# Kernel tuning notes

Hardware: AMD Instinct MI355X
Metric: run time of the kernel (lower is better)

The kernel has to match this reference:

```python
import jax, jax.numpy as jnp
import numpy as np

NEG_SLOPE = 0.2
EPS = 1e-16

N_NODES = 50000
N_EDGES = 800000
IN_CH = 128
HEADS = 4
OUT_CH = 32


def setup_inputs() -> dict:
    key = jax.random.key(0)
    k1, k2, k3, k4, k5 = jax.random.split(key, 5)
    x = jax.random.normal(k1, (N_NODES, IN_CH), dtype=jnp.float32)
    edge_index = jax.random.randint(k2, (2, N_EDGES), 0, N_NODES, dtype=jnp.int64)
    # Glorot-ish scaling for stability
    W = jax.random.normal(k3, (IN_CH, HEADS * OUT_CH), dtype=jnp.float32) / np.sqrt(IN_CH)
    att_src = jax.random.normal(k4, (HEADS, OUT_CH), dtype=jnp.float32) / np.sqrt(OUT_CH)
    att_dst = jax.random.normal(k5, (HEADS, OUT_CH), dtype=jnp.float32) / np.sqrt(OUT_CH)
    bias = jnp.zeros((HEADS * OUT_CH,), dtype=jnp.float32)
    return {"x": x, "edge_index": edge_index, "W": W,
            "att_src": att_src, "att_dst": att_dst, "bias": bias}


def reference(x, edge_index, W, att_src, att_dst, bias):
    N = x.shape[0]
    H, C = att_src.shape

    # PyG GATConv default: add self-loops
    self_loop = jnp.arange(N, dtype=edge_index.dtype)
    src = jnp.concatenate([edge_index[0], self_loop])  # [E+N]
    dst = jnp.concatenate([edge_index[1], self_loop])  # [E+N]

    # Linear transform, split heads: [N, H, C]
    h = (x @ W).reshape(N, H, C)

    # Per-node attention logits: [N, H]
    a_src = jnp.sum(h * att_src[None], axis=-1)
    a_dst = jnp.sum(h * att_dst[None], axis=-1)

    # Per-edge logits with LeakyReLU: [E+N, H]
    e = a_src[src] + a_dst[dst]
    e = jnp.where(e >= 0, e, NEG_SLOPE * e)

    # Segment softmax over destination-node neighborhoods
    e_max = jax.ops.segment_max(e, dst, num_segments=N)  # [N, H]
    e_exp = jnp.exp(e - e_max[dst])
    denom = jax.ops.segment_sum(e_exp, dst, num_segments=N)  # [N, H]
    alpha = e_exp / (denom[dst] + EPS)  # [E+N, H]

    # Weighted scatter-aggregate of messages: [N, H, C]
    msgs = h[src] * alpha[:, :, None]
    out = jax.ops.segment_sum(msgs, dst, num_segments=N)

    out = out.reshape(N, H * C) + bias  # concat heads + bias
    return jax.nn.relu(out)  # wrapper activation (dropout=0 is identity)
```

## Files before the change

kernel.cpp:

```cpp
#include <hip/hip_runtime.h>
#include <hip/hip_bf16.h>
#include <math.h>

#define NEG_SLOPE 0.2f
#define EPS_F 1e-16f
#define PCAP 4096
#define NPMAX 512

typedef float f32x4 __attribute__((ext_vector_type(4)));
typedef short bf16x8 __attribute__((ext_vector_type(8)));

__device__ __forceinline__ unsigned int pk2bf(float a, float b) {
    unsigned int ua = __float_as_uint(a), ub = __float_as_uint(b);
    ua = (ua + 0x7fffu + ((ua >> 16) & 1u)) >> 16;
    ub = (ub + 0x7fffu + ((ub >> 16) & 1u)) >> 16;
    return ua | (ub << 16);
}
__device__ __forceinline__ unsigned short f2bf(float f) {
    unsigned int u = __float_as_uint(f);
    return (unsigned short)((u + 0x7fffu + ((u >> 16) & 1u)) >> 16);
}
__device__ __forceinline__ float bf_lo(unsigned int p) { return __uint_as_float(p << 16); }
__device__ __forceinline__ float bf_hi(unsigned int p) { return __uint_as_float(p & 0xffff0000u); }

__global__ __launch_bounds__(256)
void k_front(const unsigned int* __restrict__ eidx,
             int* __restrict__ pcnt, unsigned int* __restrict__ rec, int E, int npart,
             const float* __restrict__ W,
             const float* __restrict__ att_src, const float* __restrict__ att_dst,
             unsigned short* __restrict__ Wtb, int nPB) {
    __shared__ int hist[NPMAX];
    __shared__ int base[NPMAX];
    __shared__ int sflag;
    int t = threadIdx.x;

    if ((int)blockIdx.x < nPB) {
        if (t < 64) {
            unsigned int v = eidx[2 * t + 1];
            #pragma unroll
            for (int m = 1; m <= 32; m <<= 1) v |= __shfl_xor(v, m);
            if (t == 0) sflag = (v == 0u) ? 1 : 0;
        }
        for (int p = t; p < npart; p += 256) hist[p] = 0;
        __syncthreads();
        int flag = sflag;
        const uint2* e2p = (const uint2*)eidx;
        int e0 = blockIdx.x * 4096;
        int se[16], de[16];
        #pragma unroll
        for (int i = 0; i < 16; i++) {
            int idx = e0 + t + i * 256;
            de[i] = -1;
            if (idx < E) {
                if (flag) { se[i] = (int)e2p[idx].x; de[i] = (int)e2p[E + idx].x; }
                else      { se[i] = (int)eidx[idx];  de[i] = (int)eidx[E + idx]; }
                atomicAdd(&hist[de[i] >> 7], 1);
            }
        }
        __syncthreads();
        for (int p = t; p < npart; p += 256) {
            int c = hist[p];
            base[p] = c ? atomicAdd(&pcnt[p], c) : 0;
            hist[p] = 0;
        }
        __syncthreads();
        #pragma unroll
        for (int i = 0; i < 16; i++) {
            if (de[i] >= 0) {
                int p = de[i] >> 7;
                int r = atomicAdd(&hist[p], 1);
                int pos = base[p] + r;
                if (pos < PCAP)
                    rec[(size_t)p * PCAP + pos] =
                        ((unsigned int)se[i] << 7) | (unsigned int)(de[i] & 127);
            }
        }
    } else {
        int b = (int)blockIdx.x - nPB;
        if (b < 64) {
            int id = b * 256 + t;
            int k = id >> 7, col = id & 127;
            Wtb[col * 128 + k] = f2bf(W[id]);
        } else {
            int k4 = t >> 3, j = t & 7;
            const float* att = (j < 4) ? att_src : att_dst;
            int h = j & 3;
            #pragma unroll
            for (int kk = 0; kk < 4; kk++) {
                int k = k4 * 4 + kk;
                float s = 0.f;
                #pragma unroll
                for (int c = 0; c < 32; c++)
                    s = fmaf(W[k * 128 + h * 32 + c], att[h * 32 + c], s);
                Wtb[(128 + j) * 128 + k] = f2bf(s);
            }
            for (int idx = t; idx < 1024; idx += 256)
                Wtb[(136 + (idx >> 7)) * 128 + (idx & 127)] = 0;
        }
    }
}

__global__ __launch_bounds__(256)
void k_mid(const float* __restrict__ x, const unsigned short* __restrict__ Wtb,
           unsigned short* __restrict__ hb,
           float* __restrict__ a_src, float* __restrict__ a_dst, int N,
           const int* __restrict__ pcnt, const unsigned int* __restrict__ rec,
           unsigned int* __restrict__ srt, int* __restrict__ rowArr,
           int* __restrict__ degArr, int gb) {
    __shared__ __align__(16) char smem[53248];
    int t = threadIdx.x;

    if ((int)blockIdx.x < gb) {
        unsigned short* xlds = (unsigned short*)smem;
        unsigned short* wlds = (unsigned short*)(smem + 16384);
        int l = t & 63, w = t >> 6;
        int br = blockIdx.x * 64;

        #pragma unroll
        for (int i = 0; i < 9; i++) {
            int u = t + i * 256;
            uint4 v = *(const uint4*)(Wtb + u * 8);
            int row = u >> 4;
            int e8  = (u & 15) * 8;
            *(uint4*)&wlds[row * 128 + (e8 ^ ((row & 7) << 3))] = v;
        }
        {
            int row = t >> 2, kq = t & 3;
            int gr = br + row;
            const float* xp = x + (size_t)gr * 128 + kq * 32;
            #pragma unroll
            for (int j = 0; j < 4; j++) {
                uint4 pk = make_uint4(0u, 0u, 0u, 0u);
                if (gr < N) {
                    float4 v0 = *(const float4*)(xp + j * 8);
                    float4 v1 = *(const float4*)(xp + j * 8 + 4);
                    pk.x = pk2bf(v0.x, v0.y); pk.y = pk2bf(v0.z, v0.w);
                    pk.z = pk2bf(v1.x, v1.y); pk.w = pk2bf(v1.z, v1.w);
                }
                int e8 = kq * 32 + j * 8;
                *(uint4*)&xlds[row * 128 + (e8 ^ ((row & 7) << 3))] = pk;
            }
        }
        __syncthreads();

        bf16x8 a[4];
        int arow = w * 16 + (l & 15);
        int ae   = (l >> 4) * 8;
        #pragma unroll
        for (int kc = 0; kc < 4; kc++)
            a[kc] = *(const bf16x8*)&xlds[arow * 128 + ((kc * 32 + ae) ^ ((arow & 7) << 3))];

        int rowbase = br + w * 16 + (l >> 4) * 4;

        #pragma unroll
        for (int nb = 0; nb < 9; nb++) {
            int brow = nb * 16 + (l & 15);
            f32x4 c = {0.f, 0.f, 0.f, 0.f};
            #pragma unroll
            for (int kc = 0; kc < 4; kc++) {
                bf16x8 bfr = *(const bf16x8*)&wlds[brow * 128 + ((kc * 32 + ae) ^ ((brow & 7) << 3))];
                c = __builtin_amdgcn_mfma_f32_16x16x32_bf16(a[kc], bfr, c, 0, 0, 0);
            }
            if (nb < 8) {
                #pragma unroll
                for (int r = 0; r < 4; r++) {
                    float v  = c[r];
                    float vo = __shfl_xor(v, 1);
                    int row = rowbase + r;
                    if (row < N && (l & 1) == 0)
                        *(unsigned int*)&hb[(size_t)row * 128 + nb * 16 + (l & 15)] = pk2bf(v, vo);
                }
            } else {
                int j = l & 15;
                #pragma unroll
                for (int r = 0; r < 4; r++) {
                    int row = rowbase + r;
                    if (row < N && j < 8) {
                        if (j < 4) a_src[row * 4 + j]     = c[r];
                        else       a_dst[row * 4 + j - 4] = c[r];
                    }
                }
            }
        }
    } else {
        int* hist = (int*)smem;
        int* offs = hist + 128;
        int* cur  = offs + 128;
        unsigned int* ssort = (unsigned int*)(smem + 1536);
        int p = (int)blockIdx.x - gb;
        if (t < 128) { hist[t] = 0; cur[t] = 0; }
        __syncthreads();
        int cnt = min(pcnt[p], PCAP);
        const unsigned int* rb = rec + (size_t)p * PCAP;
        for (int i = t; i < cnt; i += 256) atomicAdd(&hist[rb[i] & 127], 1);
        __syncthreads();
        if (t < 128) offs[t] = hist[t];
        __syncthreads();
        #pragma unroll
        for (int off = 1; off < 128; off <<= 1) {
            int u = (t < 128 && t >= off) ? offs[t - off] : 0;
            __syncthreads();
            if (t < 128) offs[t] += u;
            __syncthreads();
        }
        for (int i = t; i < cnt; i += 256) {
            unsigned int r = rb[i];
            int n = r & 127;
            int pos = (offs[n] - hist[n]) + atomicAdd(&cur[n], 1);
            ssort[pos] = r >> 7;
        }
        __syncthreads();
        for (int i = t; i < cnt; i += 256) srt[(size_t)p * PCAP + i] = ssort[i];
        int node = (p << 7) + t;
        if (t < 128 && node < N) {
            rowArr[node] = p * PCAP + (offs[t] - hist[t]);
            degArr[node] = hist[t];
        }
    }
}

#define BATCH4(bk, j, ad, den, ax, ay)                                          \
    {                                                                            \
        int s0=(int)bk[j], s1=(int)bk[j+1], s2=(int)bk[j+2], s3=(int)bk[j+3];    \
        float a0=a_src[s0*4+head], a1=a_src[s1*4+head];                          \
        float a2=a_src[s2*4+head], a3=a_src[s3*4+head];                          \
        unsigned int p0=*(const unsigned int*)&hb[(size_t)s0*128+c0];            \
        unsigned int p1=*(const unsigned int*)&hb[(size_t)s1*128+c0];            \
        unsigned int p2=*(const unsigned int*)&hb[(size_t)s2*128+c0];            \
        unsigned int p3=*(const unsigned int*)&hb[(size_t)s3*128+c0];            \
        float e0=a0+ad; e0=fmaxf(e0,NEG_SLOPE*e0); float w0=__expf(e0);          \
        float e1=a1+ad; e1=fmaxf(e1,NEG_SLOPE*e1); float w1=__expf(e1);          \
        float e2=a2+ad; e2=fmaxf(e2,NEG_SLOPE*e2); float w2=__expf(e2);          \
        float e3=a3+ad; e3=fmaxf(e3,NEG_SLOPE*e3); float w3=__expf(e3);          \
        den += (w0+w1)+(w2+w3);                                                  \
        ax = fmaf(w0,bf_lo(p0),ax); ay = fmaf(w0,bf_hi(p0),ay);                  \
        ax = fmaf(w1,bf_lo(p1),ax); ay = fmaf(w1,bf_hi(p1),ay);                  \
        ax = fmaf(w2,bf_lo(p2),ax); ay = fmaf(w2,bf_hi(p2),ay);                  \
        ax = fmaf(w3,bf_lo(p3),ax); ay = fmaf(w3,bf_hi(p3),ay);                  \
    }

#define ONEEDGE(bk, j, ad, den, ax, ay)                                          \
    {                                                                            \
        int s0=(int)bk[j];                                                       \
        float a0=a_src[s0*4+head];                                               \
        unsigned int p0=*(const unsigned int*)&hb[(size_t)s0*128+c0];            \
        float e0=a0+ad; e0=fmaxf(e0,NEG_SLOPE*e0); float w0=__expf(e0);          \
        den += w0;                                                               \
        ax = fmaf(w0,bf_lo(p0),ax); ay = fmaf(w0,bf_hi(p0),ay);                  \
    }

__global__ __launch_bounds__(256)
void k_aggregate(const unsigned int* __restrict__ srt, const int* __restrict__ rowArr,
                 const int* __restrict__ degArr,
                 const float* __restrict__ a_src, const float* __restrict__ a_dst,
                 const unsigned short* __restrict__ hb,
                 const float* __restrict__ bias,
                 float* __restrict__ out, int N) {
    int wave = threadIdx.x >> 6;
    int lane = threadIdx.x & 63;
    int c0 = lane * 2;
    int head = lane >> 4;
    int dA = blockIdx.x * 8 + wave * 2;
    int dB = dA + 1;
    if (dA >= N) return;
    bool vB = dB < N;

    float adA, denA, axA, ayA; const unsigned int* bkA; int gA;
    {
        adA = a_dst[dA * 4 + head];
        float es = a_src[dA * 4 + head] + adA;
        es = fmaxf(es, NEG_SLOPE * es);
        float w = __expf(es);
        unsigned int hp = *(const unsigned int*)&hb[(size_t)dA * 128 + c0];
        denA = w; axA = w * bf_lo(hp); ayA = w * bf_hi(hp);
        bkA = srt + rowArr[dA]; gA = degArr[dA];
    }
    float adB = 0.f, denB = 0.f, axB = 0.f, ayB = 0.f;
    const unsigned int* bkB = srt; int gB = 0;
    if (vB) {
        adB = a_dst[dB * 4 + head];
        float es = a_src[dB * 4 + head] + adB;
        es = fmaxf(es, NEG_SLOPE * es);
        float w = __expf(es);
        unsigned int hp = *(const unsigned int*)&hb[(size_t)dB * 128 + c0];
        denB = w; axB = w * bf_lo(hp); ayB = w * bf_hi(hp);
        bkB = srt + rowArr[dB]; gB = degArr[dB];
    }

    int jA = 0, jB = 0;
    while (jA + 4 <= gA && jB + 4 <= gB) {
        BATCH4(bkA, jA, adA, denA, axA, ayA);
        BATCH4(bkB, jB, adB, denB, axB, ayB);
        jA += 4; jB += 4;
    }
    while (jA + 4 <= gA) { BATCH4(bkA, jA, adA, denA, axA, ayA); jA += 4; }
    while (jB + 4 <= gB) { BATCH4(bkB, jB, adB, denB, axB, ayB); jB += 4; }
    while (jA < gA && jB < gB) {
        ONEEDGE(bkA, jA, adA, denA, axA, ayA);
        ONEEDGE(bkB, jB, adB, denB, axB, ayB);
        jA++; jB++;
    }
    for (; jA < gA; jA++) ONEEDGE(bkA, jA, adA, denA, axA, ayA);
    for (; jB < gB; jB++) ONEEDGE(bkB, jB, adB, denB, axB, ayB);

    float2 b2 = *(const float2*)&bias[c0];
    {
        float rden = 1.f / (denA + EPS_F);
        float ox = fmaxf(axA * rden + b2.x, 0.f);
        float oy = fmaxf(ayA * rden + b2.y, 0.f);
        *(float2*)&out[(size_t)dA * 128 + c0] = make_float2(ox, oy);
    }
    if (vB) {
        float rden = 1.f / (denB + EPS_F);
        float ox = fmaxf(axB * rden + b2.x, 0.f);
        float oy = fmaxf(ayB * rden + b2.y, 0.f);
        *(float2*)&out[(size_t)dB * 128 + c0] = make_float2(ox, oy);
    }
}

extern "C" void kernel_launch(void* const* d_in, const int* in_sizes, int n_in,
                              void* d_out, int out_size, void* d_ws, size_t ws_size,
                              hipStream_t stream) {
    const float* x        = (const float*)d_in[0];
    const unsigned int* e = (const unsigned int*)d_in[1];
    const float* W        = (const float*)d_in[2];
    const float* att_src  = (const float*)d_in[3];
    const float* att_dst  = (const float*)d_in[4];
    const float* bias     = (const float*)d_in[5];
    float* out            = (float*)d_out;

    int N = in_sizes[0] / 128;
    int E = in_sizes[1] / 2;
    int npart = (N + 127) >> 7;

    char* ws = (char*)d_ws;
    size_t off = 0;
    unsigned short* Wtb    = (unsigned short*)(ws + off); off += 144 * 128 * 2;
    unsigned short* hb     = (unsigned short*)(ws + off); off += (size_t)N * 128 * 2;
    float*          a_src  = (float*)(ws + off);          off += (size_t)N * 16;
    float*          a_dst  = (float*)(ws + off);          off += (size_t)N * 16;
    int*            rowArr = (int*)(ws + off);            off += (size_t)N * 4;
    int*            degArr = (int*)(ws + off);            off += (size_t)N * 4;
    int*            pcnt   = (int*)(ws + off);            off += (size_t)NPMAX * 4;
    unsigned int*   rec    = (unsigned int*)(ws + off);   off += (size_t)npart * PCAP * 4;
    unsigned int*   srt    = (unsigned int*)(ws + off);   off += (size_t)npart * PCAP * 4;

    int nPB = (E + 4095) / 4096;
    int gb  = (N + 63) / 64;

    hipMemsetAsync(pcnt, 0, (size_t)NPMAX * 4, stream);

    k_front<<<nPB + 65, 256, 0, stream>>>(e, pcnt, rec, E, npart,
                                          W, att_src, att_dst, Wtb, nPB);
    k_mid<<<gb + npart, 256, 0, stream>>>(x, Wtb, hb, a_src, a_dst, N,
                                          pcnt, rec, srt, rowArr, degArr, gb);
    k_aggregate<<<(N + 7) / 8, 256, 0, stream>>>(srt, rowArr, degArr,
                                                 a_src, a_dst, hb, bias, out, N);
}
```

Before: 80.98 us.

## Regroup kernels: fuse edge partitioning with GEMM, split prep and binning, use exp2

The weight preparation moves into its own small kernel. Edge partitioning now runs in the same launch as the x@W GEMM, and the per-partition counting sort becomes a separate kernel. The attention projection columns are pre-scaled by log2(e), so the aggregate kernel can call exp2f instead of __expf. This aims to overlap the memory-bound edge pass with the compute-bound GEMM, at the cost of one extra kernel launch; the bf16 rounding of the scaled logits changes slightly.

Result: slower. 87.71 us (+8.3%).

```diff
diff --git a/kernel.cpp b/kernel.cpp
--- a/kernel.cpp
+++ b/kernel.cpp
@@ -6,6 +6,7 @@
 #define EPS_F 1e-16f
 #define PCAP 4096
 #define NPMAX 512
+#define LOG2E 1.44269504088896f
 
 typedef float f32x4 __attribute__((ext_vector_type(4)));
 typedef short bf16x8 __attribute__((ext_vector_type(8)));
@@ -23,27 +24,54 @@
 __device__ __forceinline__ float bf_lo(unsigned int p) { return __uint_as_float(p << 16); }
 __device__ __forceinline__ float bf_hi(unsigned int p) { return __uint_as_float(p & 0xffff0000u); }
 
+__global__ void k_prep(const float* __restrict__ W,
+                       const float* __restrict__ att_src, const float* __restrict__ att_dst,
+                       unsigned short* __restrict__ Wtb) {
+    int b = blockIdx.x, t = threadIdx.x;
+    if (b < 64) {
+        int id = b * 256 + t;
+        int k = id >> 7, col = id & 127;
+        Wtb[col * 128 + k] = f2bf(W[id]);
+    } else {
+        int k4 = t >> 3, j = t & 7;
+        const float* att = (j < 4) ? att_src : att_dst;
+        int h = j & 3;
+        #pragma unroll
+        for (int kk = 0; kk < 4; kk++) {
+            int k = k4 * 4 + kk;
+            float s = 0.f;
+            #pragma unroll
+            for (int c = 0; c < 32; c++)
+                s = fmaf(W[k * 128 + h * 32 + c], att[h * 32 + c], s);
+            Wtb[(128 + j) * 128 + k] = f2bf(s * LOG2E);
+        }
+        for (int idx = t; idx < 1024; idx += 256)
+            Wtb[(136 + (idx >> 7)) * 128 + (idx & 127)] = 0;
+    }
+}
+
 __global__ __launch_bounds__(256)
-void k_front(const unsigned int* __restrict__ eidx,
-             int* __restrict__ pcnt, unsigned int* __restrict__ rec, int E, int npart,
-             const float* __restrict__ W,
-             const float* __restrict__ att_src, const float* __restrict__ att_dst,
-             unsigned short* __restrict__ Wtb, int nPB) {
-    __shared__ int hist[NPMAX];
-    __shared__ int base[NPMAX];
-    __shared__ int sflag;
+void k_pg(const unsigned int* __restrict__ eidx,
+          int* __restrict__ pcnt, unsigned int* __restrict__ rec, int E, int npart,
+          const float* __restrict__ x, const unsigned short* __restrict__ Wtb,
+          unsigned short* __restrict__ hb,
+          float* __restrict__ a_src, float* __restrict__ a_dst, int N, int nPB) {
+    __shared__ __align__(16) char smem[53248];
     int t = threadIdx.x;
 
     if ((int)blockIdx.x < nPB) {
+        int* hist = (int*)smem;
+        int* base = (int*)(smem + 2048);
+        int* sflagp = (int*)(smem + 4096);
         if (t < 64) {
             unsigned int v = eidx[2 * t + 1];
             #pragma unroll
             for (int m = 1; m <= 32; m <<= 1) v |= __shfl_xor(v, m);
-            if (t == 0) sflag = (v == 0u) ? 1 : 0;
+            if (t == 0) *sflagp = (v == 0u) ? 1 : 0;
         }
         for (int p = t; p < npart; p += 256) hist[p] = 0;
         __syncthreads();
-        int flag = sflag;
+        int flag = *sflagp;
         const uint2* e2p = (const uint2*)eidx;
         int e0 = blockIdx.x * 4096;
         int se[16], de[16];
@@ -76,45 +104,10 @@
             }
         }
     } else {
-        int b = (int)blockIdx.x - nPB;
-        if (b < 64) {
-            int id = b * 256 + t;
-            int k = id >> 7, col = id & 127;
-            Wtb[col * 128 + k] = f2bf(W[id]);
-        } else {
-            int k4 = t >> 3, j = t & 7;
-            const float* att = (j < 4) ? att_src : att_dst;
-            int h = j & 3;
-            #pragma unroll
-            for (int kk = 0; kk < 4; kk++) {
-                int k = k4 * 4 + kk;
-                float s = 0.f;
-                #pragma unroll
-                for (int c = 0; c < 32; c++)
-                    s = fmaf(W[k * 128 + h * 32 + c], att[h * 32 + c], s);
-                Wtb[(128 + j) * 128 + k] = f2bf(s);
-            }
-            for (int idx = t; idx < 1024; idx += 256)
-                Wtb[(136 + (idx >> 7)) * 128 + (idx & 127)] = 0;
-        }
-    }
-}
-
-__global__ __launch_bounds__(256)
-void k_mid(const float* __restrict__ x, const unsigned short* __restrict__ Wtb,
-           unsigned short* __restrict__ hb,
-           float* __restrict__ a_src, float* __restrict__ a_dst, int N,
-           const int* __restrict__ pcnt, const unsigned int* __restrict__ rec,
-           unsigned int* __restrict__ srt, int* __restrict__ rowArr,
-           int* __restrict__ degArr, int gb) {
-    __shared__ __align__(16) char smem[53248];
-    int t = threadIdx.x;
-
-    if ((int)blockIdx.x < gb) {
         unsigned short* xlds = (unsigned short*)smem;
         unsigned short* wlds = (unsigned short*)(smem + 16384);
         int l = t & 63, w = t >> 6;
-        int br = blockIdx.x * 64;
+        int br = ((int)blockIdx.x - nPB) * 64;
 
         #pragma unroll
         for (int i = 0; i < 9; i++) {
@@ -182,40 +175,45 @@
                 }
             }
         }
-    } else {
-        int* hist = (int*)smem;
-        int* offs = hist + 128;
-        int* cur  = offs + 128;
-        unsigned int* ssort = (unsigned int*)(smem + 1536);
-        int p = (int)blockIdx.x - gb;
-        if (t < 128) { hist[t] = 0; cur[t] = 0; }
-        __syncthreads();
-        int cnt = min(pcnt[p], PCAP);
-        const unsigned int* rb = rec + (size_t)p * PCAP;
-        for (int i = t; i < cnt; i += 256) atomicAdd(&hist[rb[i] & 127], 1);
-        __syncthreads();
-        if (t < 128) offs[t] = hist[t];
-        __syncthreads();
-        #pragma unroll
-        for (int off = 1; off < 128; off <<= 1) {
-            int u = (t < 128 && t >= off) ? offs[t - off] : 0;
-            __syncthreads();
-            if (t < 128) offs[t] += u;
-            __syncthreads();
-        }
-        for (int i = t; i < cnt; i += 256) {
-            unsigned int r = rb[i];
-            int n = r & 127;
-            int pos = (offs[n] - hist[n]) + atomicAdd(&cur[n], 1);
-            ssort[pos] = r >> 7;
-        }
-        __syncthreads();
-        for (int i = t; i < cnt; i += 256) srt[(size_t)p * PCAP + i] = ssort[i];
-        int node = (p << 7) + t;
-        if (t < 128 && node < N) {
-            rowArr[node] = p * PCAP + (offs[t] - hist[t]);
-            degArr[node] = hist[t];
-        }
+    }
+}
+
+__global__ __launch_bounds__(256)
+void k_bin2(const int* __restrict__ pcnt, const unsigned int* __restrict__ rec,
+            unsigned int* __restrict__ srt, int* __restrict__ rowArr,
+            int* __restrict__ degArr, int N) {
+    __shared__ int hist[128];
+    __shared__ int offs[128];
+    __shared__ int cur[128];
+    __shared__ unsigned int ssort[PCAP];
+    int p = blockIdx.x, t = threadIdx.x;
+    if (t < 128) { hist[t] = 0; cur[t] = 0; }
+    __syncthreads();
+    int cnt = min(pcnt[p], PCAP);
+    const unsigned int* rb = rec + (size_t)p * PCAP;
+    for (int i = t; i < cnt; i += 256) atomicAdd(&hist[rb[i] & 127], 1);
+    __syncthreads();
+    if (t < 128) offs[t] = hist[t];
+    __syncthreads();
+    #pragma unroll
+    for (int off = 1; off < 128; off <<= 1) {
+        int u = (t < 128 && t >= off) ? offs[t - off] : 0;
+        __syncthreads();
+        if (t < 128) offs[t] += u;
+        __syncthreads();
+    }
+    for (int i = t; i < cnt; i += 256) {
+        unsigned int r = rb[i];
+        int n = r & 127;
+        int pos = (offs[n] - hist[n]) + atomicAdd(&cur[n], 1);
+        ssort[pos] = r >> 7;
+    }
+    __syncthreads();
+    for (int i = t; i < cnt; i += 256) srt[(size_t)p * PCAP + i] = ssort[i];
+    int node = (p << 7) + t;
+    if (t < 128 && node < N) {
+        rowArr[node] = p * PCAP + (offs[t] - hist[t]);
+        degArr[node] = hist[t];
     }
 }
 
@@ -228,10 +226,10 @@
         unsigned int p1=*(const unsigned int*)&hb[(size_t)s1*128+c0];            \
         unsigned int p2=*(const unsigned int*)&hb[(size_t)s2*128+c0];            \
         unsigned int p3=*(const unsigned int*)&hb[(size_t)s3*128+c0];            \
-        float e0=a0+ad; e0=fmaxf(e0,NEG_SLOPE*e0); float w0=__expf(e0);          \
-        float e1=a1+ad; e1=fmaxf(e1,NEG_SLOPE*e1); float w1=__expf(e1);          \
-        float e2=a2+ad; e2=fmaxf(e2,NEG_SLOPE*e2); float w2=__expf(e2);          \
-        float e3=a3+ad; e3=fmaxf(e3,NEG_SLOPE*e3); float w3=__expf(e3);          \
+        float e0=a0+ad; e0=fmaxf(e0,NEG_SLOPE*e0); float w0=exp2f(e0);           \
+        float e1=a1+ad; e1=fmaxf(e1,NEG_SLOPE*e1); float w1=exp2f(e1);           \
+        float e2=a2+ad; e2=fmaxf(e2,NEG_SLOPE*e2); float w2=exp2f(e2);           \
+        float e3=a3+ad; e3=fmaxf(e3,NEG_SLOPE*e3); float w3=exp2f(e3);           \
         den += (w0+w1)+(w2+w3);                                                  \
         ax = fmaf(w0,bf_lo(p0),ax); ay = fmaf(w0,bf_hi(p0),ay);                  \
         ax = fmaf(w1,bf_lo(p1),ax); ay = fmaf(w1,bf_hi(p1),ay);                  \
@@ -244,7 +242,7 @@
         int s0=(int)bk[j];                                                       \
         float a0=a_src[s0*4+head];                                               \
         unsigned int p0=*(const unsigned int*)&hb[(size_t)s0*128+c0];            \
-        float e0=a0+ad; e0=fmaxf(e0,NEG_SLOPE*e0); float w0=__expf(e0);          \
+        float e0=a0+ad; e0=fmaxf(e0,NEG_SLOPE*e0); float w0=exp2f(e0);           \
         den += w0;                                                               \
         ax = fmaf(w0,bf_lo(p0),ax); ay = fmaf(w0,bf_hi(p0),ay);                  \
     }
@@ -270,7 +268,7 @@
         adA = a_dst[dA * 4 + head];
         float es = a_src[dA * 4 + head] + adA;
         es = fmaxf(es, NEG_SLOPE * es);
-        float w = __expf(es);
+        float w = exp2f(es);
         unsigned int hp = *(const unsigned int*)&hb[(size_t)dA * 128 + c0];
         denA = w; axA = w * bf_lo(hp); ayA = w * bf_hi(hp);
         bkA = srt + rowArr[dA]; gA = degArr[dA];
@@ -281,7 +279,7 @@
         adB = a_dst[dB * 4 + head];
         float es = a_src[dB * 4 + head] + adB;
         es = fmaxf(es, NEG_SLOPE * es);
-        float w = __expf(es);
+        float w = exp2f(es);
         unsigned int hp = *(const unsigned int*)&hb[(size_t)dB * 128 + c0];
         denB = w; axB = w * bf_lo(hp); ayB = w * bf_hi(hp);
         bkB = srt + rowArr[dB]; gB = degArr[dB];
@@ -350,10 +348,10 @@
 
     hipMemsetAsync(pcnt, 0, (size_t)NPMAX * 4, stream);
 
-    k_front<<<nPB + 65, 256, 0, stream>>>(e, pcnt, rec, E, npart,
-                                          W, att_src, att_dst, Wtb, nPB);
-    k_mid<<<gb + npart, 256, 0, stream>>>(x, Wtb, hb, a_src, a_dst, N,
-                                          pcnt, rec, srt, rowArr, degArr, gb);
+    k_prep<<<65, 256, 0, stream>>>(W, att_src, att_dst, Wtb);
+    k_pg<<<nPB + gb, 256, 0, stream>>>(e, pcnt, rec, E, npart,
+                                       x, Wtb, hb, a_src, a_dst, N, nPB);
+    k_bin2<<<npart, 256, 0, stream>>>(pcnt, rec, srt, rowArr, degArr, N);
     k_aggregate<<<(N + 7) / 8, 256, 0, stream>>>(srt, rowArr, degArr,
                                                  a_src, a_dst, hb, bias, out, N);
 }
```
